# Kernel tuning notes

Measured on AMD Instinct MI355X. Metric: run time of the kernel, lower is better.

The kernel has to match this reference:

```python
import jax, jax.numpy as jnp
import numpy as np
from jax import lax

CONF_THRESH = 0.5   # from module __init__
NMS_THRESH = 0.4    # from module __init__
TOP_K = 1000        # static pre-NMS candidate cap (JAX needs fixed shapes)

B, N, C = 16, 22743, 80  # batch, predictions (608px, 3 scales), COCO classes


def setup_inputs() -> dict:
    key = jax.random.key(0)
    # YOLOv3 raw output: [B, N, 5+C] = (cx, cy, w, h, obj, cls_0..cls_{C-1})
    v3_out = jax.random.uniform(key, (B, N, 5 + C), dtype=jnp.float32)
    return {"v3_out": v3_out}


def _xywh2xyxy(b):
    cx, cy, w, h = b[..., 0], b[..., 1], b[..., 2], b[..., 3]
    return jnp.stack([cx - w * 0.5, cy - h * 0.5, cx + w * 0.5, cy + h * 0.5], axis=-1)


def _pairwise_iou(boxes):
    # boxes: [K, 4] in xyxy -> [K, K] IoU
    x1 = jnp.maximum(boxes[:, None, 0], boxes[None, :, 0])
    y1 = jnp.maximum(boxes[:, None, 1], boxes[None, :, 1])
    x2 = jnp.minimum(boxes[:, None, 2], boxes[None, :, 2])
    y2 = jnp.minimum(boxes[:, None, 3], boxes[None, :, 3])
    inter = jnp.clip(x2 - x1, 0.0) * jnp.clip(y2 - y1, 0.0)
    area = jnp.clip(boxes[:, 2] - boxes[:, 0], 0.0) * jnp.clip(boxes[:, 3] - boxes[:, 1], 0.0)
    union = area[:, None] + area[None, :] - inter
    return inter / (union + 1e-16)


def _nms_image(pred):
    # pred: [N, 5+C]
    boxes = _xywh2xyxy(pred[:, :4])                 # [N, 4]
    obj = pred[:, 4]
    cls_conf = jnp.max(pred[:, 5:], axis=-1)        # best class confidence
    cls_id = jnp.argmax(pred[:, 5:], axis=-1)       # best class index
    # confidence filter (obj >= thresh) folded into the sort key
    score = jnp.where(obj >= CONF_THRESH, obj * cls_conf, -1.0)
    top_score, idx = lax.top_k(score, TOP_K)        # sorted descending by score
    valid = top_score > 0.0                          # survivors of the conf filter

    boxes_k = boxes[idx]          # [K, 4]
    obj_k = obj[idx]
    conf_k = cls_conf[idx]
    cls_k = cls_id[idx]

    iou = _pairwise_iou(boxes_k)                                   # [K, K]
    suppress = (iou > NMS_THRESH) & (cls_k[:, None] == cls_k[None, :])

    # greedy NMS over the score-sorted list: box i (if kept) kills later overlaps
    later = jnp.arange(TOP_K)

    def step(i, keep):
        kill = suppress[i] & (later > i) & keep[i]
        return keep & ~kill

    keep = lax.fori_loop(0, TOP_K, step, valid)

    # detections: (x1, y1, x2, y2, obj_conf, cls_conf, cls_id), zeroed where dropped
    dets = jnp.concatenate(
        [boxes_k, obj_k[:, None], conf_k[:, None], cls_k.astype(jnp.float32)[:, None]],
        axis=-1,
    )
    return dets * keep[:, None].astype(dets.dtype)   # [K, 7]


def reference(v3_out):
    # [B, K, 7] padded detections per image (zero rows = suppressed/invalid)
    return jax.vmap(_nms_image)(v3_out)
```

## Files before the change

kernel.cpp:

```cpp
#include <hip/hip_runtime.h>
#include <cstdint>

#pragma clang fp contract(off)

constexpr int cB = 16;
constexpr int cN = 22743;
constexpr int cROW = 85;
constexpr int cK = 1000;
constexpr float CONF_T = 0.5f;
constexpr float NMS_T = 0.4f;

__global__ __launch_bounds__(256) void k_score(const float* __restrict__ in,
                                               unsigned* __restrict__ ukey) {
  __shared__ float sdata[10880];
  constexpr int F4_PER_BLK = 2720;
  constexpr int TOTAL_F4 = (cB * cN * cROW) / 4;
  int tid = threadIdx.x;
  const float4* gin4 = (const float4*)in;
  float4* s4 = (float4*)sdata;
  int base_f4 = blockIdx.x * F4_PER_BLK;
#pragma unroll
  for (int q = 0; q < 11; ++q) {
    int k = tid + 256 * q;
    if (k < F4_PER_BLK) {
      int g = base_f4 + k;
      if (g < TOTAL_F4) s4[k] = gin4[g];
    }
  }
  __syncthreads();
  if (tid < 128) {
    int r = blockIdx.x * 128 + tid;
    if (r < cB * cN) {
      const float* rowp = sdata + cROW * tid;
      float obj = rowp[4];
      float m = rowp[5];
#pragma unroll
      for (int j = 6; j < 85; ++j) m = fmaxf(m, rowp[j]);
      unsigned u = 0u;
      if (obj >= CONF_T) {
        float s = obj * m;
        if (s > 0.0f) u = __float_as_uint(s);
      }
      ukey[r] = u;
    }
  }
}

__device__ __forceinline__ void sort1024_u32_asc(unsigned* a, int tid) {
  for (int k = 2; k <= 1024; k <<= 1) {
    for (int j = k >> 1; j >= 1; j >>= 1) {
      __syncthreads();
      if (tid < 512) {
        int i = ((tid & ~(j - 1)) << 1) | (tid & (j - 1));
        int p = i | j;
        unsigned x = a[i], y = a[p];
        bool up = ((i & k) == 0);
        bool sw = up ? (x > y) : (x < y);
        if (sw) { a[i] = y; a[p] = x; }
      }
    }
  }
  __syncthreads();
}

__global__ __launch_bounds__(1024) void k_topk(const unsigned* __restrict__ ukey,
                                               int* __restrict__ topidx) {
  __shared__ unsigned hist[2048];
  __shared__ unsigned psum[1024];
  __shared__ unsigned long long cand[1024];
  __shared__ unsigned eqbuf[1024];
  __shared__ unsigned sh_T, sh_newrank, sh_E, sh_cnt;
  int img = blockIdx.x;
  int tid = threadIdx.x;
  int lane = tid & 63;
  const unsigned* uk = ukey + (size_t)img * cN;

  unsigned prefix = 0;
  int bits = 0;
  unsigned rank = cK;
  unsigned gtc = 0;
  unsigned E = 0;

  for (int r = 0; r < 3; ++r) {
    int nb = (r < 2) ? 11 : 10;
    int shift = 32 - bits - nb;
    hist[tid] = 0u; hist[tid + 1024] = 0u;
    __syncthreads();
    for (int i0 = 0; i0 < cN; i0 += 1024) {
      int i = i0 + tid;
      unsigned u = (i < cN) ? uk[i] : 0u;
      bool inr = (i < cN);
      bool match = inr && (bits == 0 || (u >> (32 - bits)) == prefix);
      bool isz = match && (u == 0u);
      bool nz = match && (u != 0u);
      unsigned long long mz = __ballot(isz);
      if (isz && lane == (__ffsll((long long)mz) - 1))
        atomicAdd(&hist[0], (unsigned)__popcll(mz));
      if (nz) atomicAdd(&hist[(u >> shift) & ((1u << nb) - 1u)], 1u);
    }
    __syncthreads();
    unsigned h0 = hist[2 * tid];
    unsigned h1 = hist[2 * tid + 1];
    psum[tid] = h0 + h1;
    __syncthreads();
    for (int s = 1; s < 1024; s <<= 1) {
      unsigned v = psum[tid] + ((tid + s < 1024) ? psum[tid + s] : 0u);
      __syncthreads();
      psum[tid] = v;
      __syncthreads();
    }
    unsigned St = psum[tid];
    unsigned Stn = (tid < 1023) ? psum[tid + 1] : 0u;
    unsigned sufE = St;
    unsigned sufO = St - h0;
    if (sufE >= rank && sufO < rank) { sh_T = 2u * tid; sh_newrank = rank - sufO; sh_E = h0; }
    if (sufO >= rank && Stn < rank) { sh_T = 2u * tid + 1u; sh_newrank = rank - Stn; sh_E = h1; }
    __syncthreads();
    unsigned T = sh_T;
    unsigned nr = sh_newrank;
    E = sh_E;
    gtc += rank - nr;
    rank = nr;
    prefix = (prefix << nb) | T;
    bits += nb;
    __syncthreads();
    if (gtc + E <= 1024u) break;
  }

  bool tiepath = (gtc + E > 1024u);
  unsigned pivotLo = (bits >= 32) ? prefix : (prefix << (32 - bits));
  cand[tid] = (unsigned long long)tid;
  eqbuf[tid] = 0xFFFFFFFFu;
  if (tid == 0) sh_cnt = 0u;
  __syncthreads();

  if (!tiepath) {
    for (int i0 = 0; i0 < cN; i0 += 1024) {
      int i = i0 + tid;
      unsigned u = (i < cN) ? uk[i] : 0u;
      bool m = (i < cN) && (u >= pivotLo);
      unsigned long long mb = __ballot(m);
      if (m) {
        int ldr = __ffsll((long long)mb) - 1;
        unsigned base = 0;
        if (lane == ldr) base = atomicAdd(&sh_cnt, (unsigned)__popcll(mb));
        base = __shfl(base, ldr);
        unsigned pos = base + (unsigned)__popcll(mb & ((1ull << lane) - 1ull));
        if (pos < 1024u)
          cand[pos] = ((unsigned long long)u << 32) |
                      (unsigned long long)(0xFFFFFFFFu - (unsigned)i);
      }
    }
    __syncthreads();
  } else {
    unsigned P = prefix;
    for (int i0 = 0; i0 < cN; i0 += 1024) {
      int i = i0 + tid;
      unsigned u = (i < cN) ? uk[i] : 0u;
      bool gt = (i < cN) && (u > P);
      unsigned long long mb = __ballot(gt);
      if (gt) {
        int ldr = __ffsll((long long)mb) - 1;
        unsigned base = 0;
        if (lane == ldr) base = atomicAdd(&sh_cnt, (unsigned)__popcll(mb));
        base = __shfl(base, ldr);
        unsigned pos = base + (unsigned)__popcll(mb & ((1ull << lane) - 1ull));
        if (pos < 1024u)
          cand[pos] = ((unsigned long long)u << 32) |
                      (unsigned long long)(0xFFFFFFFFu - (unsigned)i);
      }
      bool eq = (i < cN) && (u == P);
      if (eq) {
        unsigned pe = atomicAdd(&sh_E, 0u);
        (void)pe;
      }
    }
    __syncthreads();
    if (tid == 0) sh_E = 0u;
    __syncthreads();
    for (int i0 = 0; i0 < cN; i0 += 1024) {
      int i = i0 + tid;
      unsigned u = (i < cN) ? uk[i] : 0u;
      bool eq = (i < cN) && (u == P);
      unsigned long long mb = __ballot(eq);
      if (eq) {
        int ldr = __ffsll((long long)mb) - 1;
        unsigned base = 0;
        if (lane == ldr) base = atomicAdd(&sh_E, (unsigned)__popcll(mb));
        base = __shfl(base, ldr);
        unsigned pos = base + (unsigned)__popcll(mb & ((1ull << lane) - 1ull));
        if (pos < 1024u) eqbuf[pos] = (unsigned)i;
      }
    }
    __syncthreads();
    sort1024_u32_asc(eqbuf, tid);
    int need = (int)cK - (int)gtc;
    for (int t = tid; t < need; t += 1024) {
      unsigned idx = eqbuf[t];
      if (idx != 0xFFFFFFFFu)
        cand[gtc + (unsigned)t] = ((unsigned long long)P << 32) |
                                  (unsigned long long)(0xFFFFFFFFu - idx);
    }
    __syncthreads();
  }

  unsigned long long my = cand[tid];
  unsigned rk = 0;
#pragma unroll 8
  for (int j = 0; j < 1024; ++j) rk += (cand[j] > my) ? 1u : 0u;
  if (rk < (unsigned)cK) {
    unsigned uhi = (unsigned)(my >> 32);
    int idx = (int)(0xFFFFFFFFu - (unsigned)(my & 0xFFFFFFFFull));
    topidx[img * cK + (int)rk] = (uhi > 0u) ? idx : -1;
  }
}

__global__ __launch_bounds__(256) void k_gather(const float* __restrict__ in,
                                                const int* __restrict__ topidx,
                                                float4* __restrict__ boxes,
                                                float* __restrict__ area,
                                                float* __restrict__ objv,
                                                float* __restrict__ confv,
                                                int* __restrict__ clsv,
                                                int* __restrict__ validv) {
  int wid = (int)((blockIdx.x * 256u + threadIdx.x) >> 6);
  int lane = threadIdx.x & 63;
  if (wid >= cB * cK) return;
  int img = wid / cK;
  int idx = topidx[wid];
  if (idx < 0) {
    if (lane == 0) {
      boxes[wid] = make_float4(0.f, 0.f, 0.f, 0.f);
      area[wid] = 0.f; objv[wid] = 0.f; confv[wid] = 0.f;
      clsv[wid] = -1; validv[wid] = 0;
    }
    return;
  }
  const float* row = in + ((size_t)img * cN + (size_t)idx) * cROW;
  float v = row[5 + lane];
  int ci = lane;
  if (lane < 16) {
    float v2 = row[69 + lane];
    if (v2 > v) { v = v2; ci = 64 + lane; }
  }
#pragma unroll
  for (int m = 1; m < 64; m <<= 1) {
    float ov = __shfl_xor(v, m);
    int oc = __shfl_xor(ci, m);
    if (ov > v || (ov == v && oc < ci)) { v = ov; ci = oc; }
  }
  if (lane == 0) {
    float cx = row[0], cy = row[1], w = row[2], h = row[3], ob = row[4];
    float hw = w * 0.5f, hh = h * 0.5f;
    float x1 = cx - hw, y1 = cy - hh, x2 = cx + hw, y2 = cy + hh;
    boxes[wid] = make_float4(x1, y1, x2, y2);
    area[wid] = fmaxf(x2 - x1, 0.f) * fmaxf(y2 - y1, 0.f);
    objv[wid] = ob; confv[wid] = v; clsv[wid] = ci; validv[wid] = 1;
  }
}

__global__ __launch_bounds__(256) void k_suppress(const float4* __restrict__ boxes,
                                                  const float* __restrict__ area,
                                                  const int* __restrict__ clsv,
                                                  unsigned* __restrict__ St) {
  __shared__ float sx1[1056], sy1[1056], sx2[1056], sy2[1056], sar[1056];
  __shared__ int scls[1056];
  int img = blockIdx.x >> 7;
  int rb = (blockIdx.x & 127) * 8;
  int tid = threadIdx.x;
  for (int i = tid; i < 1024; i += 256) {
    int p = i + (i >> 5);
    if (i < cK) {
      float4 b = boxes[img * cK + i];
      sx1[p] = b.x; sy1[p] = b.y; sx2[p] = b.z; sy2[p] = b.w;
      sar[p] = area[img * cK + i];
      scls[p] = clsv[img * cK + i];
    } else {
      sx1[p] = 0.f; sy1[p] = 0.f; sx2[p] = 0.f; sy2[p] = 0.f; sar[p] = 0.f;
      scls[p] = -2;
    }
  }
  __syncthreads();
  int i = rb + (tid >> 5);
  int w = tid & 31;
  int pi = i + (i >> 5);
  float bx1 = sx1[pi], by1 = sy1[pi], bx2 = sx2[pi], by2 = sy2[pi], ba = sar[pi];
  int bc = scls[pi];
  unsigned word = 0u;
#pragma unroll 4
  for (int bit = 0; bit < 32; ++bit) {
    int pj = 33 * w + bit;
    float xx1 = fmaxf(bx1, sx1[pj]);
    float yy1 = fmaxf(by1, sy1[pj]);
    float xx2 = fminf(bx2, sx2[pj]);
    float yy2 = fminf(by2, sy2[pj]);
    float inter = fmaxf(xx2 - xx1, 0.f) * fmaxf(yy2 - yy1, 0.f);
    float uni = ba + sar[pj] - inter;
    float iou = inter / (uni + 1e-16f);
    if (iou > NMS_T && bc == scls[pj]) word |= (1u << bit);
  }
  St[((size_t)(img * 32 + w)) * 1024 + (size_t)i] = word;
}

__device__ __forceinline__ unsigned u4c(const uint4& v, int c) {
  return c == 0 ? v.x : c == 1 ? v.y : c == 2 ? v.z : v.w;
}

__device__ __forceinline__ void nms_load(const uint4* __restrict__ colv, int b,
                                         uint4 (&buf)[8]) {
#pragma unroll
  for (int q = 0; q < 8; ++q) buf[q] = colv[8 * b + q];
}

__device__ __forceinline__ void nms_proc(int b, int lane, unsigned& kw,
                                         const uint4 (&W)[8]) {
  unsigned dec = 0u;
  if (lane == b) {
    unsigned kwb = kw;
#pragma unroll
    for (int t = 0; t < 32; ++t) {
      if ((kwb >> t) & 1u) {
        dec |= (1u << t);
        unsigned rw = u4c(W[t >> 2], t & 3);
        unsigned mgt = (t == 31) ? 0u : (0xFFFFFFFFu << (t + 1));
        kwb &= ~(rw & mgt);
      }
    }
    kw = kwb;
  }
  dec = __shfl(dec, b);
  if (lane > b) {
#pragma unroll
    for (int t = 0; t < 32; ++t) {
      unsigned sel = 0u - ((dec >> t) & 1u);
      kw &= ~(u4c(W[t >> 2], t & 3) & sel);
    }
  }
}

__global__ __launch_bounds__(64) void k_nms(const unsigned* __restrict__ St,
                                            const int* __restrict__ validv,
                                            const float4* __restrict__ boxes,
                                            const float* __restrict__ objv,
                                            const float* __restrict__ confv,
                                            const int* __restrict__ clsv,
                                            float* __restrict__ out) {
  __shared__ unsigned keep_sh[32];
  int img = blockIdx.x;
  int lane = threadIdx.x;
  if (lane < 32) {
    const uint4* colv = (const uint4*)(St + ((size_t)(img * 32 + lane)) * 1024);
    unsigned kw = 0u;
    for (int b = 0; b < 32; ++b) {
      int k = (lane << 5) + b;
      if (k < cK && validv[img * cK + k]) kw |= (1u << b);
    }
    uint4 bufA[8], bufB[8];
    nms_load(colv, 0, bufA);
    for (int b = 0; b < 32; b += 2) {
      if (b + 1 < 32) nms_load(colv, b + 1, bufB);
      nms_proc(b, lane, kw, bufA);
      if (b + 2 < 32) nms_load(colv, b + 2, bufA);
      nms_proc(b + 1, lane, kw, bufB);
    }
    keep_sh[lane] = kw;
  }
  __syncthreads();
  for (int k = lane; k < cK; k += 64) {
    bool kp = ((keep_sh[k >> 5] >> (k & 31)) & 1u) != 0u;
    size_t o = ((size_t)img * cK + (size_t)k) * 7;
    if (kp) {
      float4 b = boxes[img * cK + k];
      out[o + 0] = b.x; out[o + 1] = b.y; out[o + 2] = b.z; out[o + 3] = b.w;
      out[o + 4] = objv[img * cK + k];
      out[o + 5] = confv[img * cK + k];
      out[o + 6] = (float)clsv[img * cK + k];
    } else {
      out[o + 0] = 0.f; out[o + 1] = 0.f; out[o + 2] = 0.f; out[o + 3] = 0.f;
      out[o + 4] = 0.f; out[o + 5] = 0.f; out[o + 6] = 0.f;
    }
  }
}

extern "C" void kernel_launch(void* const* d_in, const int* in_sizes, int n_in,
                              void* d_out, int out_size, void* d_ws, size_t ws_size,
                              hipStream_t stream) {
  const float* in = (const float*)d_in[0];
  float* out = (float*)d_out;
  char* ws = (char*)d_ws;
  size_t off = 0;
  auto take = [&](size_t bytes) {
    size_t r = off;
    off += (bytes + 255) & ~(size_t)255;
    return r;
  };
  unsigned* ukey = (unsigned*)(ws + take((size_t)cB * cN * 4));
  int* topidx = (int*)(ws + take((size_t)cB * cK * 4));
  float4* boxes = (float4*)(ws + take((size_t)cB * cK * 16));
  float* area = (float*)(ws + take((size_t)cB * cK * 4));
  float* objv = (float*)(ws + take((size_t)cB * cK * 4));
  float* confv = (float*)(ws + take((size_t)cB * cK * 4));
  int* clsv = (int*)(ws + take((size_t)cB * cK * 4));
  int* validv = (int*)(ws + take((size_t)cB * cK * 4));
  unsigned* St = (unsigned*)(ws + take((size_t)cB * 32 * 1024 * 4));

  int nrows = cB * cN;
  int blocks1 = (nrows + 127) / 128;
  k_score<<<blocks1, 256, 0, stream>>>(in, ukey);
  k_topk<<<cB, 1024, 0, stream>>>(ukey, topidx);
  int waves3 = cB * cK;
  k_gather<<<(waves3 * 64 + 255) / 256, 256, 0, stream>>>(in, topidx, boxes, area,
                                                          objv, confv, clsv, validv);
  k_suppress<<<cB * 128, 256, 0, stream>>>(boxes, area, clsv, St);
  k_nms<<<cB, 64, 0, stream>>>(St, validv, boxes, objv, confv, clsv, out);
}
```

Measured before the change: 284.7 us.

## Split class-max across thread pairs and use wave-shuffle suffix scan in top-k

The score kernel now assigns two threads per row, each reducing 40 class scores with four independent max accumulators, then combines the halves with a lane shuffle, so all 256 threads work instead of 128. The top-k radix-select replaces a 10-step shared-memory Hillis-Steele scan, which needed two barriers per step, with an intra-wavefront shuffle suffix scan plus a 16-entry cross-wave total. A dead atomicAdd(&sh_E,0) loop in the tie path is also removed. Bank conflicts on the strided 85-float row reads may change with the new two-threads-per-row access pattern.

After: 281.8 us. No clear change (-1.0%).

```diff
diff --git a/kernel.cpp b/kernel.cpp
--- a/kernel.cpp
+++ b/kernel.cpp
@@ -28,20 +28,30 @@
     }
   }
   __syncthreads();
-  if (tid < 128) {
-    int r = blockIdx.x * 128 + tid;
-    if (r < cB * cN) {
-      const float* rowp = sdata + cROW * tid;
+  int r = tid >> 1, h = tid & 1;
+  int grow = blockIdx.x * 128 + r;
+  if (grow < cB * cN) {
+    const float* rowp = sdata + cROW * r;
+    int j0 = 5 + h * 40;
+    float m0 = rowp[j0 + 0], m1 = rowp[j0 + 1];
+    float m2 = rowp[j0 + 2], m3 = rowp[j0 + 3];
+#pragma unroll
+    for (int k = 4; k < 40; k += 4) {
+      m0 = fmaxf(m0, rowp[j0 + k + 0]);
+      m1 = fmaxf(m1, rowp[j0 + k + 1]);
+      m2 = fmaxf(m2, rowp[j0 + k + 2]);
+      m3 = fmaxf(m3, rowp[j0 + k + 3]);
+    }
+    float m = fmaxf(fmaxf(m0, m1), fmaxf(m2, m3));
+    m = fmaxf(m, __shfl_xor(m, 1));
+    if (h == 0) {
       float obj = rowp[4];
-      float m = rowp[5];
-#pragma unroll
-      for (int j = 6; j < 85; ++j) m = fmaxf(m, rowp[j]);
       unsigned u = 0u;
       if (obj >= CONF_T) {
         float s = obj * m;
         if (s > 0.0f) u = __float_as_uint(s);
       }
-      ukey[r] = u;
+      ukey[grow] = u;
     }
   }
 }
@@ -66,13 +76,14 @@
 __global__ __launch_bounds__(1024) void k_topk(const unsigned* __restrict__ ukey,
                                                int* __restrict__ topidx) {
   __shared__ unsigned hist[2048];
-  __shared__ unsigned psum[1024];
+  __shared__ unsigned wtot[16];
   __shared__ unsigned long long cand[1024];
   __shared__ unsigned eqbuf[1024];
   __shared__ unsigned sh_T, sh_newrank, sh_E, sh_cnt;
   int img = blockIdx.x;
   int tid = threadIdx.x;
   int lane = tid & 63;
+  int wv = tid >> 6;
   const unsigned* uk = ukey + (size_t)img * cN;
 
   unsigned prefix = 0;
@@ -101,20 +112,21 @@
     __syncthreads();
     unsigned h0 = hist[2 * tid];
     unsigned h1 = hist[2 * tid + 1];
-    psum[tid] = h0 + h1;
-    __syncthreads();
-    for (int s = 1; s < 1024; s <<= 1) {
-      unsigned v = psum[tid] + ((tid + s < 1024) ? psum[tid + s] : 0u);
-      __syncthreads();
-      psum[tid] = v;
-      __syncthreads();
-    }
-    unsigned St = psum[tid];
-    unsigned Stn = (tid < 1023) ? psum[tid + 1] : 0u;
-    unsigned sufE = St;
-    unsigned sufO = St - h0;
-    if (sufE >= rank && sufO < rank) { sh_T = 2u * tid; sh_newrank = rank - sufO; sh_E = h0; }
-    if (sufO >= rank && Stn < rank) { sh_T = 2u * tid + 1u; sh_newrank = rank - Stn; sh_E = h1; }
+    unsigned s2 = h0 + h1;
+#pragma unroll
+    for (int s = 1; s < 64; s <<= 1) {
+      unsigned t = __shfl_down(s2, s);
+      s2 += (lane + s < 64) ? t : 0u;
+    }
+    if (lane == 0) wtot[wv] = s2;
+    __syncthreads();
+    unsigned above = 0;
+    for (int w2 = wv + 1; w2 < 16; ++w2) above += wtot[w2];
+    unsigned S_even = above + s2;
+    unsigned S_odd = S_even - h0;
+    unsigned S_next = S_odd - h1;
+    if (S_even >= rank && S_odd < rank) { sh_T = 2u * tid; sh_newrank = rank - S_odd; sh_E = h0; }
+    if (S_odd >= rank && S_next < rank) { sh_T = 2u * tid + 1u; sh_newrank = rank - S_next; sh_E = h1; }
     __syncthreads();
     unsigned T = sh_T;
     unsigned nr = sh_newrank;
@@ -168,11 +180,6 @@
         if (pos < 1024u)
           cand[pos] = ((unsigned long long)u << 32) |
                       (unsigned long long)(0xFFFFFFFFu - (unsigned)i);
-      }
-      bool eq = (i < cN) && (u == P);
-      if (eq) {
-        unsigned pe = atomicAdd(&sh_E, 0u);
-        (void)pe;
       }
     }
     __syncthreads();
```
